# Kernel tuning notes

Measured on AMD Instinct MI355X. Metric: run time of the kernel, lower is better.

The kernel has to match this reference:

```python
import jax, jax.numpy as jnp
import numpy as np

N_NODES = 40000
N_EDGES = 640000
D = 128
BN_EPS = 1e-5
GATE_EPS = 1e-6


def _linear_params(key, d_in, d_out):
    kw, kb = jax.random.split(key)
    bound = 1.0 / np.sqrt(d_in)
    W = jax.random.uniform(kw, (d_out, d_in), jnp.float32, -bound, bound)
    b = jax.random.uniform(kb, (d_out,), jnp.float32, -bound, bound)
    return W, b


def setup_inputs() -> dict:
    key = jax.random.key(0)
    ks = jax.random.split(key, 8)
    x = jax.random.normal(ks[0], (N_NODES, D), jnp.float32)
    edge_index = jax.random.randint(ks[1], (2, N_EDGES), 0, N_NODES, jnp.int64)
    edge_attr = jax.random.normal(ks[2], (N_EDGES, D), jnp.float32)
    W_src_gate, b_src_gate = _linear_params(ks[3], D, D)
    W_dst_gate, b_dst_gate = _linear_params(ks[4], D, D)
    W_edge_gate, b_edge_gate = _linear_params(ks[5], D, D)
    W_src_update, b_src_update = _linear_params(ks[6], D, D)
    W_dst_update, b_dst_update = _linear_params(ks[7], D, D)
    return dict(
        x=x, edge_index=edge_index, edge_attr=edge_attr,
        W_src_gate=W_src_gate, b_src_gate=b_src_gate,
        W_dst_gate=W_dst_gate, b_dst_gate=b_dst_gate,
        W_edge_gate=W_edge_gate, b_edge_gate=b_edge_gate,
        W_src_update=W_src_update, b_src_update=b_src_update,
        W_dst_update=W_dst_update, b_dst_update=b_dst_update,
        bn_nodes_gamma=jnp.ones((D,), jnp.float32), bn_nodes_beta=jnp.zeros((D,), jnp.float32),
        bn_edges_gamma=jnp.ones((D,), jnp.float32), bn_edges_beta=jnp.zeros((D,), jnp.float32),
    )


def _batch_norm(z, gamma, beta):
    # training-mode BN: batch mean, biased variance (torch semantics)
    mean = jnp.mean(z, axis=0)
    var = jnp.mean(jnp.square(z - mean), axis=0)
    return gamma * (z - mean) * jax.lax.rsqrt(var + BN_EPS) + beta


def reference(x, edge_index, edge_attr,
              W_src_gate, b_src_gate, W_dst_gate, b_dst_gate,
              W_edge_gate, b_edge_gate, W_src_update, b_src_update,
              W_dst_update, b_dst_update,
              bn_nodes_gamma, bn_nodes_beta, bn_edges_gamma, bn_edges_beta):
    row, col = edge_index[0], edge_index[1]
    num_nodes = x.shape[0]
    x_row = x[row]                      # [E, D] gather
    x_col = x[col]                      # [E, D] gather
    e_src = x_row @ W_src_gate.T + b_src_gate
    e_dst = x_col @ W_dst_gate.T + b_dst_gate
    m = e_src + e_dst + edge_attr @ W_edge_gate.T + b_edge_gate  # [E, D]
    sigma = jax.nn.sigmoid(m)
    h_weighted = (x_col @ W_dst_update.T + b_dst_update) * sigma
    h_sum = jax.ops.segment_sum(h_weighted, col, num_segments=num_nodes)
    sigma_sum = jax.ops.segment_sum(sigma, col, num_segments=num_nodes)
    h_normalized = h_sum / (sigma_sum + GATE_EPS)
    x_new = x @ W_src_update.T + b_src_update + h_normalized
    x_new = jax.nn.softplus(_batch_norm(x_new, bn_nodes_gamma, bn_nodes_beta))
    y_new = jax.nn.softplus(_batch_norm(m, bn_edges_gamma, bn_edges_beta))
    x_new = x + x_new          # residual
    y_new = edge_attr + y_new  # residual
    return (x_new, y_new)
```

## Files before the change

kernel.cpp:

```cpp
#include <hip/hip_runtime.h>

#define NN 40000
#define NE 640000

typedef unsigned short u16;
typedef unsigned int u32;
typedef __attribute__((ext_vector_type(4))) float f32x4;
typedef __attribute__((ext_vector_type(4))) float fv4;
typedef __attribute__((ext_vector_type(4))) u32 uv4;
typedef __attribute__((ext_vector_type(8))) __bf16 bf16x8;

#define LSTR 132
#define TPW 4

__device__ __forceinline__ float bf2f(u16 u) { return __uint_as_float(((u32)u) << 16); }
__device__ __forceinline__ u16 f2bf(float f) {
  u32 u = __float_as_uint(f);
  u32 r = 0x7fffu + ((u >> 16) & 1u);
  return (u16)((u + r) >> 16);
}
__device__ __forceinline__ float splus(float v) {
  return fmaxf(v, 0.0f) + __logf(1.0f + __expf(-fabsf(v)));
}
__device__ __forceinline__ fv4 ntl4(const float* p) {
  return __builtin_nontemporal_load((const fv4*)p);
}

__global__ void sniff_k(const u32* __restrict__ gamma, const u32* __restrict__ eidx,
                        u32* __restrict__ flags) {
  if (threadIdx.x == 0) {
    flags[0] = (gamma[0] == 0x3F803F80u) ? 1u : 0u;
    u32 odd = eidx[1] | eidx[3] | eidx[5] | eidx[7] |
              eidx[9] | eidx[11] | eidx[13] | eidx[15];
    flags[1] = (odd == 0u) ? 1u : 0u;
  }
}

__device__ __forceinline__ int load_col(const void* eidx, int e, u32 i64) {
  int nc = i64 ? (int)((const u32*)eidx)[2 * ((size_t)NE + e)]
               : ((const int*)eidx)[NE + e];
  return min(max(nc, 0), NN - 1);
}
__device__ __forceinline__ int load_row(const void* eidx, int e, u32 i64) {
  int nr = i64 ? (int)((const u32*)eidx)[2 * (size_t)e]
               : ((const int*)eidx)[e];
  return min(max(nr, 0), NN - 1);
}

__global__ __launch_bounds__(256) void wconv5_k(
    const float* __restrict__ W0, const float* __restrict__ W1,
    const float* __restrict__ W2, const float* __restrict__ W3,
    const float* __restrict__ W4, u16* __restrict__ out) {
  int i = blockIdx.x * 256 + threadIdx.x;
  int mtx = blockIdx.y;
  const float* W = (mtx == 0) ? W0 : (mtx == 1) ? W1 : (mtx == 2) ? W2
                 : (mtx == 3) ? W3 : W4;
  out[mtx * 16384 + i] = f2bf(W[i]);
}

__global__ __launch_bounds__(256) void hist_k(const void* __restrict__ eidx,
                                              u32* __restrict__ cnt,
                                              const u32* __restrict__ flags) {
  int e = blockIdx.x * 256 + threadIdx.x;
  atomicAdd(&cnt[load_col(eidx, e, flags[1])], 1u);
}

__device__ __forceinline__ bf16x8 a_frag(const float* __restrict__ row, int kbase) {
  float4 f0 = *(const float4*)(row + kbase);
  float4 f1 = *(const float4*)(row + kbase + 4);
  bf16x8 a;
  a[0] = (__bf16)f0.x; a[1] = (__bf16)f0.y; a[2] = (__bf16)f0.z; a[3] = (__bf16)f0.w;
  a[4] = (__bf16)f1.x; a[5] = (__bf16)f1.y; a[6] = (__bf16)f1.z; a[7] = (__bf16)f1.w;
  return a;
}

__device__ __forceinline__ bf16x8 cvt8v(fv4 a, fv4 b) {
  bf16x8 r;
  r[0] = (__bf16)a[0]; r[1] = (__bf16)a[1]; r[2] = (__bf16)a[2]; r[3] = (__bf16)a[3];
  r[4] = (__bf16)b[0]; r[5] = (__bf16)b[1]; r[6] = (__bf16)b[2]; r[7] = (__bf16)b[3];
  return r;
}

__device__ __forceinline__ void gemm16(const bf16x8 af[4], const u16* __restrict__ Wb,
                                       const float* __restrict__ bias, int lane,
                                       f32x4 acc[8]) {
  int l15 = lane & 15, lk = lane >> 4;
#pragma unroll
  for (int n = 0; n < 8; ++n) {
    float bv = bias[n * 16 + l15];
    acc[n] = (f32x4){bv, bv, bv, bv};
  }
#pragma unroll
  for (int n = 0; n < 8; ++n) {
    const u16* bp = Wb + (size_t)(n * 16 + l15) * 128 + lk * 8;
#pragma unroll
    for (int k = 0; k < 4; ++k) {
      bf16x8 b = *(const bf16x8*)(bp + 32 * k);
      acc[n] = __builtin_amdgcn_mfma_f32_16x16x32_bf16(af[k], b, acc[n], 0, 0, 0);
    }
  }
}

__device__ __forceinline__ void store_tile(u16* __restrict__ out, int m0, int lane,
                                           const f32x4 acc[8]) {
  int l15 = lane & 15, lk = lane >> 4;
#pragma unroll
  for (int n = 0; n < 8; ++n)
#pragma unroll
    for (int r = 0; r < 4; ++r)
      out[(size_t)(m0 + lk * 4 + r) * 128 + n * 16 + l15] = f2bf(acc[n][r]);
}

__global__ __launch_bounds__(256) void node_gemm_k(
    const float* __restrict__ x, const u16* __restrict__ Wb,
    const float* __restrict__ B0, const float* __restrict__ B1,
    const float* __restrict__ B2, const float* __restrict__ B3,
    const u32* __restrict__ cnt,
    u16* __restrict__ o0, u16* __restrict__ o1,
    u16* __restrict__ o2, u16* __restrict__ o3,
    float* __restrict__ statsg) {
  __shared__ float red[256];
  int tid = threadIdx.x, lane = tid & 63, w = tid >> 6;
  for (int i = tid; i < 256; i += 256) red[i] = 0.f;
  __syncthreads();
  int m0 = blockIdx.x * 64 + w * 16;
  int l15 = lane & 15, lk = lane >> 4;
  const float* arow = x + (size_t)(m0 + l15) * 128;
  bf16x8 af[4];
#pragma unroll
  for (int k = 0; k < 4; ++k) af[k] = a_frag(arow, 32 * k + 8 * lk);
  f32x4 acc[8], accd[8];
  gemm16(af, Wb + 0 * 16384, B0, lane, acc);  store_tile(o0, m0, lane, acc);
  gemm16(af, Wb + 1 * 16384, B1, lane, acc);  store_tile(o1, m0, lane, acc);
  gemm16(af, Wb + 2 * 16384, B2, lane, accd); store_tile(o2, m0, lane, accd);
  gemm16(af, Wb + 3 * 16384, B3, lane, acc);  store_tile(o3, m0, lane, acc);
  float g[4];
#pragma unroll
  for (int r = 0; r < 4; ++r) g[r] = (cnt[m0 + lk * 4 + r] != 0u) ? 1.0f : 0.0f;
#pragma unroll
  for (int n = 0; n < 8; ++n) {
    float a1 = 0.f, a2 = 0.f;
#pragma unroll
    for (int r = 0; r < 4; ++r) {
      float zv = acc[n][r] + g[r] * accd[n][r];
      a1 += zv;
      a2 = fmaf(zv, zv, a2);
    }
    a1 += __shfl_xor(a1, 16); a1 += __shfl_xor(a1, 32);
    a2 += __shfl_xor(a2, 16); a2 += __shfl_xor(a2, 32);
    if (lk == 0) {
      atomicAdd(&red[n * 16 + l15], a1);
      atomicAdd(&red[128 + n * 16 + l15], a2);
    }
  }
  __syncthreads();
  for (int i = tid; i < 256; i += 256) atomicAdd(&statsg[256 + i], red[i]);
}

__global__ __launch_bounds__(256, 2) void edge_gemm_k(
    const float* __restrict__ ea, const u16* __restrict__ Wgb,
    const float* __restrict__ Bg,
    const u16* __restrict__ g_src, const u16* __restrict__ g_dst,
    const void* __restrict__ eidx,
    u16* __restrict__ mge, float* __restrict__ statsg,
    const u32* __restrict__ flags) {
  __shared__ __align__(16) u16 mt[4][16][LSTR];
  __shared__ __align__(16) float gt[4][16][LSTR];
  int tid = threadIdx.x, lane = tid & 63, w = tid >> 6;
  int l15 = lane & 15, lk = lane >> 4;
  int el = lane >> 2, c4 = lane & 3;
  u32 i64 = flags[1];

  bf16x8 bf[8][4];
#pragma unroll
  for (int n = 0; n < 8; ++n)
#pragma unroll
    for (int k = 0; k < 4; ++k)
      bf[n][k] = *(const bf16x8*)(Wgb + (size_t)(n * 16 + l15) * 128 + lk * 8 + 32 * k);
  float bias[8];
#pragma unroll
  for (int n = 0; n < 8; ++n) bias[n] = Bg[n * 16 + l15];

  float e1[8] = {0.f, 0.f, 0.f, 0.f, 0.f, 0.f, 0.f, 0.f};
  float e2[8] = {0.f, 0.f, 0.f, 0.f, 0.f, 0.f, 0.f, 0.f};

  int base = (blockIdx.x * 4 + w) * (TPW * 16);
  const float* aptr = ea + (size_t)(base + l15) * 128 + 8 * lk;

  int rowc = load_row(eidx, base + el, i64);
  int colc = load_col(eidx, base + el, i64);
  uv4 gsv[4], gdv[4];
#pragma unroll
  for (int it = 0; it < 4; ++it) {
    gsv[it] = *(const uv4*)(g_src + (size_t)rowc * 128 + c4 * 8 + it * 32);
    gdv[it] = *(const uv4*)(g_dst + (size_t)colc * 128 + c4 * 8 + it * 32);
  }
  fv4 tmp[8];
#pragma unroll
  for (int k = 0; k < 4; ++k) {
    tmp[2 * k]     = ntl4(aptr + 32 * k);
    tmp[2 * k + 1] = ntl4(aptr + 32 * k + 4);
  }
  bf16x8 af[4];
#pragma unroll
  for (int k = 0; k < 4; ++k) af[k] = cvt8v(tmp[2 * k], tmp[2 * k + 1]);
  int rown = load_row(eidx, base + 16 + el, i64);
  int coln = load_col(eidx, base + 16 + el, i64);

  for (int t = 0; t < TPW; ++t) {
#pragma unroll
    for (int it = 0; it < 4; ++it) {
      int ch = c4 + 4 * it;
      const u16* sp = (const u16*)&gsv[it];
      const u16* dp = (const u16*)&gdv[it];
      fv4 lo, hi;
#pragma unroll
      for (int j = 0; j < 4; ++j) lo[j] = bf2f(sp[j]) + bf2f(dp[j]);
#pragma unroll
      for (int j = 0; j < 4; ++j) hi[j] = bf2f(sp[4 + j]) + bf2f(dp[4 + j]);
      *(fv4*)&gt[w][el][ch * 8]     = lo;
      *(fv4*)&gt[w][el][ch * 8 + 4] = hi;
    }
    if (t + 1 < TPW) {
      const float* anx = aptr + (size_t)(t + 1) * 16 * 128;
#pragma unroll
      for (int k = 0; k < 4; ++k) {
        tmp[2 * k]     = ntl4(anx + 32 * k);
        tmp[2 * k + 1] = ntl4(anx + 32 * k + 4);
      }
    }
    if (t + 1 < TPW) {
#pragma unroll
      for (int it = 0; it < 4; ++it) {
        gsv[it] = *(const uv4*)(g_src + (size_t)rown * 128 + c4 * 8 + it * 32);
        gdv[it] = *(const uv4*)(g_dst + (size_t)coln * 128 + c4 * 8 + it * 32);
      }
    }
    int rn2 = rown, cn2 = coln;
    if (t + 2 < TPW) {
      rn2 = load_row(eidx, base + (t + 2) * 16 + el, i64);
      cn2 = load_col(eidx, base + (t + 2) * 16 + el, i64);
    }
    f32x4 acc[8];
#pragma unroll
    for (int n = 0; n < 8; ++n)
      acc[n] = (f32x4){bias[n], bias[n], bias[n], bias[n]};
#pragma unroll
    for (int n = 0; n < 8; ++n)
#pragma unroll
      for (int k = 0; k < 4; ++k)
        acc[n] = __builtin_amdgcn_mfma_f32_16x16x32_bf16(af[k], bf[n][k], acc[n], 0, 0, 0);
#pragma unroll
    for (int n = 0; n < 8; ++n) {
#pragma unroll
      for (int r = 0; r < 4; ++r) {
        float mv = acc[n][r] + gt[w][lk * 4 + r][n * 16 + l15];
        e1[n] += mv;
        e2[n] = fmaf(mv, mv, e2[n]);
        mt[w][lk * 4 + r][n * 16 + l15] = f2bf(mv);
      }
    }
    int e0 = base + t * 16;
#pragma unroll
    for (int it = 0; it < 4; ++it) {
      int ch = c4 + 4 * it;
      uv4 v = *(const uv4*)&mt[w][el][ch * 8];
      __builtin_nontemporal_store(v, (uv4*)(mge + (size_t)(e0 + el) * 128 + ch * 8));
    }
    if (t + 1 < TPW) {
#pragma unroll
      for (int k = 0; k < 4; ++k) af[k] = cvt8v(tmp[2 * k], tmp[2 * k + 1]);
    }
    rown = rn2; coln = cn2;
  }
#pragma unroll
  for (int n = 0; n < 8; ++n) {
    float s1 = e1[n], s2 = e2[n];
    s1 += __shfl_xor(s1, 16); s1 += __shfl_xor(s1, 32);
    s2 += __shfl_xor(s2, 16); s2 += __shfl_xor(s2, 32);
    if (lk == 0) {
      atomicAdd(&statsg[n * 16 + l15], s1);
      atomicAdd(&statsg[128 + n * 16 + l15], s2);
    }
  }
}

__global__ void stats_fin_k(const float* __restrict__ es1, const float* __restrict__ es2,
                            const float* __restrict__ ns1, const float* __restrict__ ns2,
                            const float* __restrict__ eg_, const float* __restrict__ eb_,
                            const float* __restrict__ ng_, const float* __restrict__ nb_,
                            float* __restrict__ params) {
  int d = threadIdx.x;
  float em = es1[d] * (1.0f / NE);
  float ev = fmaxf(es2[d] * (1.0f / NE) - em * em, 0.0f);
  float esc = eg_[d] * rsqrtf(ev + 1e-5f);
  params[d] = esc;
  params[128 + d] = eb_[d] - em * esc;
  float nm = ns1[d] * (1.0f / NN);
  float nv = fmaxf(ns2[d] * (1.0f / NN) - nm * nm, 0.0f);
  float nsc = ng_[d] * rsqrtf(nv + 1e-5f);
  params[256 + d] = nsc;
  params[384 + d] = nb_[d] - nm * nsc;
}

__global__ __launch_bounds__(256) void node_fin2_k(
    const float* __restrict__ x, const u16* __restrict__ us,
    const u16* __restrict__ ud, const u32* __restrict__ cnt,
    const float* __restrict__ params, float* __restrict__ out) {
  size_t t = (size_t)blockIdx.x * 256 + threadIdx.x;
  size_t base = t * 8;
  int d0 = (int)(base & 127);
  int n = (int)(t >> 4);
  float g = (cnt[n] != 0u) ? 1.0f : 0.0f;
  float4 xa = *(const float4*)(x + base);
  float4 xb = *(const float4*)(x + base + 4);
  float xv[8] = {xa.x, xa.y, xa.z, xa.w, xb.x, xb.y, xb.z, xb.w};
  uint4 usv = *(const uint4*)(us + base);
  uint4 udv = *(const uint4*)(ud + base);
  const u16* up = (const u16*)&usv;
  const u16* dp = (const u16*)&udv;
  float o[8];
#pragma unroll
  for (int j = 0; j < 8; ++j) {
    float z = bf2f(up[j]) + g * bf2f(dp[j]);
    float bnv = z * params[256 + d0 + j] + params[384 + d0 + j];
    o[j] = xv[j] + splus(bnv);
  }
  *(float4*)(out + base) = make_float4(o[0], o[1], o[2], o[3]);
  *(float4*)(out + base + 4) = make_float4(o[4], o[5], o[6], o[7]);
}

__global__ __launch_bounds__(256) void edge_fin_k(
    const float* __restrict__ edge_attr, const u16* __restrict__ mge,
    const float* __restrict__ params, float* __restrict__ out) {
  size_t t = (size_t)blockIdx.x * 256 + threadIdx.x;
  size_t base = t * 8;
  int d0 = (int)(base & 127);
  float4 ea = *(const float4*)(edge_attr + base);
  float4 eb = *(const float4*)(edge_attr + base + 4);
  float ev[8] = {ea.x, ea.y, ea.z, ea.w, eb.x, eb.y, eb.z, eb.w};
  uint4 mv_ = *(const uint4*)(mge + base);
  const u16* mp = (const u16*)&mv_;
  float o[8];
#pragma unroll
  for (int j = 0; j < 8; ++j) {
    float m = bf2f(mp[j]);
    float bnv = m * params[d0 + j] + params[128 + d0 + j];
    o[j] = ev[j] + splus(bnv);
  }
  *(float4*)(out + base) = make_float4(o[0], o[1], o[2], o[3]);
  *(float4*)(out + base + 4) = make_float4(o[4], o[5], o[6], o[7]);
}

extern "C" void kernel_launch(void* const* d_in, const int* in_sizes, int n_in,
                              void* d_out, int out_size, void* d_ws, size_t ws_size,
                              hipStream_t stream) {
  const float* x        = (const float*)d_in[0];
  const void*  eidx     = d_in[1];
  const float* edge_att = (const float*)d_in[2];
  const float* Wsg = (const float*)d_in[3];  const float* bsg = (const float*)d_in[4];
  const float* Wdg = (const float*)d_in[5];  const float* bdg = (const float*)d_in[6];
  const float* Weg = (const float*)d_in[7];  const float* beg = (const float*)d_in[8];
  const float* Wsu = (const float*)d_in[9];  const float* bsu = (const float*)d_in[10];
  const float* Wdu = (const float*)d_in[11]; const float* bdu = (const float*)d_in[12];
  const float* bng = (const float*)d_in[13]; const float* bnb = (const float*)d_in[14];
  const float* beg_g = (const float*)d_in[15]; const float* beb = (const float*)d_in[16];

  char* ws = (char*)d_ws;
  u16*   g_src  = (u16*)(ws + 0);
  u16*   g_dst  = (u16*)(ws + 10240000);
  u16*   u_dst  = (u16*)(ws + 20480000);
  u16*   u_src  = (u16*)(ws + 30720000);
  float* stats  = (float*)(ws + 40960000);
  u32*   flags  = (u32*)(ws + 40964096);
  u16*   wbuf   = (u16*)(ws + 40968192);
  u32*   cnt    = (u32*)(ws + 41132032);
  u16*   mge    = (u16*)(ws + 41292032);

  hipMemsetAsync(stats, 0, 4096, stream);
  hipMemsetAsync(cnt, 0, 160000, stream);

  sniff_k<<<1, 64, 0, stream>>>((const u32*)bng, (const u32*)eidx, flags);
  wconv5_k<<<dim3(64, 5), 256, 0, stream>>>(Wsg, Wdg, Wdu, Wsu, Weg, wbuf);
  hist_k<<<NE / 256, 256, 0, stream>>>(eidx, cnt, flags);
  node_gemm_k<<<NN / 64, 256, 0, stream>>>(x, wbuf, bsg, bdg, bdu, bsu, cnt,
                                           g_src, g_dst, u_dst, u_src, stats);
  edge_gemm_k<<<NE / (64 * TPW), 256, 0, stream>>>(edge_att, wbuf + 4 * 16384, beg,
                                                   g_src, g_dst, eidx,
                                                   mge, stats, flags);
  stats_fin_k<<<1, 128, 0, stream>>>(stats, stats + 128, stats + 256, stats + 384,
                                     beg_g, beb, bng, bnb, stats + 512);
  node_fin2_k<<<(NN * 128) / 2048, 256, 0, stream>>>(x, u_src, u_dst, cnt,
                                                     stats + 512, (float*)d_out);
  edge_fin_k<<<(NE * 128) / 2048, 256, 0, stream>>>(edge_att, mge, stats + 512,
                                                    (float*)d_out + (size_t)NN * 128);
}
```

Measured before the change: 583.6 us.

## Stage edge-gate weights in swizzled LDS and double edges per wave

The edge GEMM kernel now copies the bf16 gate weight matrix into XOR-swizzled shared memory and reads the B fragments from LDS on each MFMA, where before it held them in 128 registers. This frees registers for occupancy. It also aliases the gather and output staging buffers into one per-wave region, drops the two-stage prefetch of node indices and gathered rows in favour of loading them inline, and swaps nontemporal loads and stores for ordinary ones. TPW rises from 4 to 8, so each wave handles twice as many edge tiles and the grid is halved. In exchange there is more LDS traffic per MFMA and gather latency is less hidden, and the grid size must match TPW elsewhere in the code.

```diff
diff --git a/kernel.cpp b/kernel.cpp
--- a/kernel.cpp
+++ b/kernel.cpp
@@ -11,7 +11,7 @@
 typedef __attribute__((ext_vector_type(8))) __bf16 bf16x8;
 
 #define LSTR 132
-#define TPW 4
+#define TPW 8
 
 __device__ __forceinline__ float bf2f(u16 u) { return __uint_as_float(((u32)u) << 16); }
 __device__ __forceinline__ u16 f2bf(float f) {
@@ -21,9 +21,6 @@
 }
 __device__ __forceinline__ float splus(float v) {
   return fmaxf(v, 0.0f) + __logf(1.0f + __expf(-fabsf(v)));
-}
-__device__ __forceinline__ fv4 ntl4(const float* p) {
-  return __builtin_nontemporal_load((const fv4*)p);
 }
 
 __global__ void sniff_k(const u32* __restrict__ gamma, const u32* __restrict__ eidx,
@@ -164,19 +161,30 @@
     const void* __restrict__ eidx,
     u16* __restrict__ mge, float* __restrict__ statsg,
     const u32* __restrict__ flags) {
-  __shared__ __align__(16) u16 mt[4][16][LSTR];
-  __shared__ __align__(16) float gt[4][16][LSTR];
+  __shared__ __align__(16) char gbuf[4][16 * LSTR * 4];
+  __shared__ __align__(16) u16 Wl[16384];
   int tid = threadIdx.x, lane = tid & 63, w = tid >> 6;
   int l15 = lane & 15, lk = lane >> 4;
   int el = lane >> 2, c4 = lane & 3;
   u32 i64 = flags[1];
 
-  bf16x8 bf[8][4];
-#pragma unroll
-  for (int n = 0; n < 8; ++n)
-#pragma unroll
-    for (int k = 0; k < 4; ++k)
-      bf[n][k] = *(const bf16x8*)(Wgb + (size_t)(n * 16 + l15) * 128 + lk * 8 + 32 * k);
+  {
+    const u32* Wg32 = (const u32*)Wgb;
+    u32* Wl32 = (u32*)Wl;
+#pragma unroll
+    for (int j = 0; j < 32; ++j) {
+      int i2 = tid + 256 * j;
+      int r = i2 >> 6, c2 = i2 & 63;
+      int g = c2 >> 2, win = c2 & 3;
+      Wl32[r * 64 + (((g ^ ((r & 7) << 1)) << 2) | win)] = Wg32[i2];
+    }
+  }
+  __syncthreads();
+
+  float* gt = (float*)gbuf[w];
+  u16*   mt = (u16*)gbuf[w];
+  int sw = (l15 & 7) << 1;
+
   float bias[8];
 #pragma unroll
   for (int n = 0; n < 8; ++n) bias[n] = Bg[n * 16 + l15];
@@ -187,91 +195,82 @@
   int base = (blockIdx.x * 4 + w) * (TPW * 16);
   const float* aptr = ea + (size_t)(base + l15) * 128 + 8 * lk;
 
-  int rowc = load_row(eidx, base + el, i64);
-  int colc = load_col(eidx, base + el, i64);
-  uv4 gsv[4], gdv[4];
-#pragma unroll
-  for (int it = 0; it < 4; ++it) {
-    gsv[it] = *(const uv4*)(g_src + (size_t)rowc * 128 + c4 * 8 + it * 32);
-    gdv[it] = *(const uv4*)(g_dst + (size_t)colc * 128 + c4 * 8 + it * 32);
-  }
   fv4 tmp[8];
 #pragma unroll
   for (int k = 0; k < 4; ++k) {
-    tmp[2 * k]     = ntl4(aptr + 32 * k);
-    tmp[2 * k + 1] = ntl4(aptr + 32 * k + 4);
+    tmp[2 * k]     = *(const fv4*)(aptr + 32 * k);
+    tmp[2 * k + 1] = *(const fv4*)(aptr + 32 * k + 4);
   }
   bf16x8 af[4];
 #pragma unroll
   for (int k = 0; k < 4; ++k) af[k] = cvt8v(tmp[2 * k], tmp[2 * k + 1]);
-  int rown = load_row(eidx, base + 16 + el, i64);
-  int coln = load_col(eidx, base + 16 + el, i64);
 
   for (int t = 0; t < TPW; ++t) {
+    int e0 = base + t * 16;
+    int eg = e0 + el;
+    int grow = load_row(eidx, eg, i64);
+    int gcol = load_col(eidx, eg, i64);
+#pragma unroll
+    for (int it = 0; it < 4; ++it) {
+      uv4 gsv = *(const uv4*)(g_src + (size_t)grow * 128 + c4 * 8 + it * 32);
+      uv4 gdv = *(const uv4*)(g_dst + (size_t)gcol * 128 + c4 * 8 + it * 32);
+      const u16* sp = (const u16*)&gsv;
+      const u16* dp = (const u16*)&gdv;
+      fv4 lo, hi;
+#pragma unroll
+      for (int j = 0; j < 4; ++j) lo[j] = bf2f(sp[j]) + bf2f(dp[j]);
+#pragma unroll
+      for (int j = 0; j < 4; ++j) hi[j] = bf2f(sp[4 + j]) + bf2f(dp[4 + j]);
+      int ch = c4 + 4 * it;
+      *(fv4*)(gt + el * LSTR + ch * 8)     = lo;
+      *(fv4*)(gt + el * LSTR + ch * 8 + 4) = hi;
+    }
+    if (t + 1 < TPW) {
+      const float* anx = aptr + (size_t)(t + 1) * 16 * 128;
+#pragma unroll
+      for (int k = 0; k < 4; ++k) {
+        tmp[2 * k]     = *(const fv4*)(anx + 32 * k);
+        tmp[2 * k + 1] = *(const fv4*)(anx + 32 * k + 4);
+      }
+    }
+    f32x4 acc[8];
+#pragma unroll
+    for (int n = 0; n < 8; ++n)
+      acc[n] = (f32x4){bias[n], bias[n], bias[n], bias[n]};
+#pragma unroll
+    for (int n = 0; n < 8; ++n)
+#pragma unroll
+      for (int k = 0; k < 4; ++k) {
+        bf16x8 b = *(const bf16x8*)(Wl + ((n * 16 + l15) << 7) +
+                                    (((lk + 4 * k) ^ sw) << 3));
+        acc[n] = __builtin_amdgcn_mfma_f32_16x16x32_bf16(af[k], b, acc[n], 0, 0, 0);
+      }
+    float g32[8][4];
+#pragma unroll
+    for (int n = 0; n < 8; ++n)
+#pragma unroll
+      for (int r = 0; r < 4; ++r)
+        g32[n][r] = gt[(lk * 4 + r) * LSTR + n * 16 + l15];
+    __builtin_amdgcn_sched_barrier(0);
+#pragma unroll
+    for (int n = 0; n < 8; ++n)
+#pragma unroll
+      for (int r = 0; r < 4; ++r) {
+        float mv = acc[n][r] + g32[n][r];
+        e1[n] += mv;
+        e2[n] = fmaf(mv, mv, e2[n]);
+        mt[(lk * 4 + r) * LSTR + n * 16 + l15] = f2bf(mv);
+      }
+    if (t + 1 < TPW) {
+#pragma unroll
+      for (int k = 0; k < 4; ++k) af[k] = cvt8v(tmp[2 * k], tmp[2 * k + 1]);
+    }
 #pragma unroll
     for (int it = 0; it < 4; ++it) {
       int ch = c4 + 4 * it;
-      const u16* sp = (const u16*)&gsv[it];
-      const u16* dp = (const u16*)&gdv[it];
-      fv4 lo, hi;
-#pragma unroll
-      for (int j = 0; j < 4; ++j) lo[j] = bf2f(sp[j]) + bf2f(dp[j]);
-#pragma unroll
-      for (int j = 0; j < 4; ++j) hi[j] = bf2f(sp[4 + j]) + bf2f(dp[4 + j]);
-      *(fv4*)&gt[w][el][ch * 8]     = lo;
-      *(fv4*)&gt[w][el][ch * 8 + 4] = hi;
-    }
-    if (t + 1 < TPW) {
-      const float* anx = aptr + (size_t)(t + 1) * 16 * 128;
-#pragma unroll
-      for (int k = 0; k < 4; ++k) {
-        tmp[2 * k]     = ntl4(anx + 32 * k);
-        tmp[2 * k + 1] = ntl4(anx + 32 * k + 4);
-      }
-    }
-    if (t + 1 < TPW) {
-#pragma unroll
-      for (int it = 0; it < 4; ++it) {
-        gsv[it] = *(const uv4*)(g_src + (size_t)rown * 128 + c4 * 8 + it * 32);
-        gdv[it] = *(const uv4*)(g_dst + (size_t)coln * 128 + c4 * 8 + it * 32);
-      }
-    }
-    int rn2 = rown, cn2 = coln;
-    if (t + 2 < TPW) {
-      rn2 = load_row(eidx, base + (t + 2) * 16 + el, i64);
-      cn2 = load_col(eidx, base + (t + 2) * 16 + el, i64);
-    }
-    f32x4 acc[8];
-#pragma unroll
-    for (int n = 0; n < 8; ++n)
-      acc[n] = (f32x4){bias[n], bias[n], bias[n], bias[n]};
-#pragma unroll
-    for (int n = 0; n < 8; ++n)
-#pragma unroll
-      for (int k = 0; k < 4; ++k)
-        acc[n] = __builtin_amdgcn_mfma_f32_16x16x32_bf16(af[k], bf[n][k], acc[n], 0, 0, 0);
-#pragma unroll
-    for (int n = 0; n < 8; ++n) {
-#pragma unroll
-      for (int r = 0; r < 4; ++r) {
-        float mv = acc[n][r] + gt[w][lk * 4 + r][n * 16 + l15];
-        e1[n] += mv;
-        e2[n] = fmaf(mv, mv, e2[n]);
-        mt[w][lk * 4 + r][n * 16 + l15] = f2bf(mv);
-      }
-    }
-    int e0 = base + t * 16;
-#pragma unroll
-    for (int it = 0; it < 4; ++it) {
-      int ch = c4 + 4 * it;
-      uv4 v = *(const uv4*)&mt[w][el][ch * 8];
-      __builtin_nontemporal_store(v, (uv4*)(mge + (size_t)(e0 + el) * 128 + ch * 8));
-    }
-    if (t + 1 < TPW) {
-#pragma unroll
-      for (int k = 0; k < 4; ++k) af[k] = cvt8v(tmp[2 * k], tmp[2 * k + 1]);
-    }
-    rown = rn2; coln = cn2;
+      uint4 v = *(const uint4*)(mt + el * LSTR + ch * 8);
+      *(uint4*)(mge + (size_t)(e0 + el) * 128 + ch * 8) = v;
+    }
   }
 #pragma unroll
   for (int n = 0; n < 8; ++n) {
```

After: 473.0 us. 18.9% less time.
